# Optimization experiments

Hardware: AMD Instinct MI355X
Metric: run time of the kernel (lower is better)

The kernel has to match this reference:

```python
import jax, jax.numpy as jnp
import numpy as np

N, K, H, T = 65536, 8, 128, 4  # nodes, max children, h_size, n_types


def setup_inputs() -> dict:
    key = jax.random.key(0)
    ks = jax.random.split(key, 8)
    h = jax.random.normal(ks[0], (N, K, H), jnp.float32)          # mailbox child hidden states
    c = jax.random.normal(ks[1], (N, K, H), jnp.float32)          # mailbox child cell states
    f_input = jax.random.normal(ks[2], (N, H), jnp.float32)       # precomputed x @ W_f per node
    type_id = jax.random.randint(ks[3], (N,), 0, T, jnp.int32)    # node type for dispatch
    scale = 0.05
    U_iou = jax.random.normal(ks[4], (T, H, 3 * H), jnp.float32) * scale  # per-type i,o,u recurrent mats
    b_iou = jax.random.normal(ks[5], (T, 3 * H), jnp.float32) * scale
    U_f = jax.random.normal(ks[6], (T, H, H), jnp.float32) * scale        # per-type forget-gate mat
    b_f = jax.random.normal(ks[7], (T, H), jnp.float32) * scale
    return dict(h=h, c=c, f_input=f_input, type_id=type_id,
                U_iou=U_iou, b_iou=b_iou, U_f=U_f, b_f=b_f)


def reference(h, c, f_input, type_id, U_iou, b_iou, U_f, b_f):
    """TypedTreeCell.reduce_func: per-type TreeLSTM child aggregation.

    Returns concat([iou_aggr, c_aggr], -1) of shape [N, 4*H].
    """
    n_types = U_iou.shape[0]
    n_nodes = h.shape[0]
    h_size = h.shape[2]
    h_sum = h.sum(axis=1)  # [N, H] child-sum for i,o,u gates
    iou_aggr = jnp.zeros((n_nodes, 3 * h_size), h.dtype)
    c_aggr = jnp.zeros((n_nodes, h_size), h.dtype)
    for t in range(n_types):  # fixed small type loop mirrors the module's dispatch
        m = (type_id == t)[:, None]
        iou_t = h_sum @ U_iou[t] + b_iou[t]                                  # [N, 3H]
        f_t = jax.nn.sigmoid(f_input[:, None, :] + h @ U_f[t] + b_f[t])     # [N, K, H]
        c_t = (f_t * c).sum(axis=1)                                          # [N, H]
        iou_aggr = jnp.where(m, iou_t, iou_aggr)
        c_aggr = jnp.where(m, c_t, c_aggr)
    return jnp.concatenate([iou_aggr, c_aggr], axis=-1)
```

## Files before the change

kernel.cpp:

```cpp
#include <hip/hip_runtime.h>
#include <cstdint>


typedef __bf16 bf16;
typedef bf16 bf16x8 __attribute__((ext_vector_type(8)));
typedef bf16 bf16x4 __attribute__((ext_vector_type(4)));
typedef float f32x4 __attribute__((ext_vector_type(4)));

#define N_NODES 65536
#define KCH 8
#define HSZ 128
#define T_TYPES 4
#define TM 16
#define LDS_STRIDE 136

#define WS_PERM_OFF   256
#define WS_PREUF_OFF  (WS_PERM_OFF + 4*N_NODES)
#define WS_PREUIOU_OFF (WS_PREUF_OFF + 131072)

__global__ void k_count(const int* __restrict__ ta, int* __restrict__ ws_i) {
    int i = blockIdx.x * blockDim.x + threadIdx.x;
    int t = ta[i];
    int lane = threadIdx.x & 63;
    #pragma unroll
    for (int tt = 0; tt < T_TYPES; ++tt) {
        unsigned long long m = __ballot(t == tt);
        int leader = __ffsll((unsigned long long)m) - 1;
        if (t == tt && lane == leader)
            atomicAdd(&ws_i[tt], (int)__popcll(m));
    }
}

__global__ void k_offsets(int* ws_i) {
    if (threadIdx.x == 0 && blockIdx.x == 0) {
        int acc = 0, tacc = 0;
        for (int t = 0; t < T_TYPES; ++t) {
            int cnt = ws_i[t];
            ws_i[8 + t] = acc;
            ws_i[4 + t] = acc;
            ws_i[12 + t] = tacc;
            acc += cnt;
            tacc += (cnt + TM - 1) / TM;
        }
        ws_i[16] = tacc;
    }
}

__global__ void k_scatter(const int* __restrict__ ta, int* __restrict__ ws_i,
                          int* __restrict__ perm) {
    int i = blockIdx.x * blockDim.x + threadIdx.x;
    int t = ta[i];
    int lane = threadIdx.x & 63;
    #pragma unroll
    for (int tt = 0; tt < T_TYPES; ++tt) {
        unsigned long long m = __ballot(t == tt);
        if (t == tt) {
            int leader = __ffsll((unsigned long long)m) - 1;
            int base = 0;
            if (lane == leader) base = atomicAdd(&ws_i[4 + tt], (int)__popcll(m));
            base = __shfl(base, leader, 64);
            int rank = (int)__popcll(m & ((1ull << lane) - 1ull));
            perm[base + rank] = i;
        }
    }
}

__global__ void k_swz(const float* __restrict__ Uf, const float* __restrict__ Uiou,
                      bf16* __restrict__ dstf, bf16* __restrict__ dstiou) {
    int idx = blockIdx.x * blockDim.x + threadIdx.x;
    if (idx < T_TYPES * HSZ * HSZ) {
        int t = idx >> 14;
        int r = (idx >> 7) & 127;
        int j = idx & 127;
        float v = Uf[idx];
        int kblk = r >> 5, kin = r & 31;
        int lane = ((kin >> 3) << 4) | (j & 15);
        int e = kin & 7;
        int cb = j >> 4;
        dstf[((((t * 4 + kblk) * 8 + cb) * 64 + lane) << 3) + e] = (bf16)v;
    } else {
        int i2 = idx - T_TYPES * HSZ * HSZ;
        int t = i2 / 49152;
        int rm = i2 - t * 49152;
        int r = rm / 384;
        int j = rm - r * 384;
        float v = Uiou[i2];
        int kblk = r >> 5, kin = r & 31;
        int lane = ((kin >> 3) << 4) | (j & 15);
        int e = kin & 7;
        int cb = j >> 4;
        dstiou[((((t * 4 + kblk) * 24 + cb) * 64 + lane) << 3) + e] = (bf16)v;
    }
}

__global__ __launch_bounds__(512, 6) void k_main(
    const float* __restrict__ h, const float* __restrict__ c,
    const float* __restrict__ f_input,
    const float* __restrict__ b_iou, const float* __restrict__ b_f,
    const int* __restrict__ perm, const int* __restrict__ ws_i,
    const bf16* __restrict__ preUf, const bf16* __restrict__ preUiou,
    float* __restrict__ out)
{
    const int b = blockIdx.x;
    if (b >= ws_i[16]) return;
    int t;
    if (b < ws_i[13]) t = 0;
    else if (b < ws_i[14]) t = 1;
    else if (b < ws_i[15]) t = 2;
    else t = 3;
    const int tile = b - ws_i[12 + t];
    const int cnt = ws_i[t];
    const int base = ws_i[8 + t] + tile * TM;
    const int rem = min(TM, cnt - tile * TM);

    __shared__ __align__(16) bf16 hs[(128 + 16) * LDS_STRIDE];
    __shared__ int gn_lds[TM];
    bf16* hsum = hs + 128 * LDS_STRIDE;

    const int tid = threadIdx.x;
    const int w2 = tid >> 6;
    const int l = tid & 63;
    const int lu = l & 15;
    const int g = l >> 4;

    {
        int node = w2 * 2 + (g >> 1);
        int khalf = (g & 1) * 4;
        int mc = node < rem ? node : 0;
        int gn = perm[base + mc];
        if (lu == 0 && (g & 1) == 0) gn_lds[node] = gn;
        const float* hp = h + (long)gn * (KCH * HSZ) + lu * 8;
        float sarr[8];
        #pragma unroll
        for (int i = 0; i < 8; ++i) sarr[i] = 0.f;
        #pragma unroll
        for (int k0 = 0; k0 < 4; ++k0) {
            int k = khalf + k0;
            const float4* p = (const float4*)(hp + k * HSZ);
            float4 a = p[0], bb = p[1];
            sarr[0] += a.x; sarr[1] += a.y; sarr[2] += a.z; sarr[3] += a.w;
            sarr[4] += bb.x; sarr[5] += bb.y; sarr[6] += bb.z; sarr[7] += bb.w;
            bf16x8 v;
            v[0] = (bf16)a.x; v[1] = (bf16)a.y; v[2] = (bf16)a.z; v[3] = (bf16)a.w;
            v[4] = (bf16)bb.x; v[5] = (bf16)bb.y; v[6] = (bf16)bb.z; v[7] = (bf16)bb.w;
            *((bf16x8*)&hs[(node * KCH + k) * LDS_STRIDE + lu * 8]) = v;
        }
        #pragma unroll
        for (int i = 0; i < 8; ++i) sarr[i] += __shfl_xor(sarr[i], 16, 64);
        if ((g & 1) == 0) {
            bf16x8 sv;
            #pragma unroll
            for (int i = 0; i < 8; ++i) sv[i] = (bf16)sarr[i];
            *((bf16x8*)&hsum[node * LDS_STRIDE + lu * 8]) = sv;
        }
    }
    __syncthreads();

    f32x4 acc[4][2];
    #pragma unroll
    for (int rt = 0; rt < 4; ++rt)
        #pragma unroll
        for (int cb = 0; cb < 2; ++cb)
            acc[rt][cb] = (f32x4){0.f, 0.f, 0.f, 0.f};

    const int rbase = (w2 >> 2) * 4;
    const int cpair = (w2 & 3);
    const bf16x8* Bf = (const bf16x8*)preUf;
    #pragma unroll
    for (int kb = 0; kb < 4; ++kb) {
        bf16x8 b0 = Bf[((t * 4 + kb) * 8 + cpair * 2 + 0) * 64 + l];
        bf16x8 b1 = Bf[((t * 4 + kb) * 8 + cpair * 2 + 1) * 64 + l];
        #pragma unroll
        for (int rt = 0; rt < 4; ++rt) {
            bf16x8 a = *((const bf16x8*)&hs[((rbase + rt) * 16 + lu) * LDS_STRIDE + kb * 32 + g * 8]);
            acc[rt][0] = __builtin_amdgcn_mfma_f32_16x16x32_bf16(a, b0, acc[rt][0], 0, 0, 0);
            acc[rt][1] = __builtin_amdgcn_mfma_f32_16x16x32_bf16(a, b1, acc[rt][1], 0, 0, 0);
        }
    }

    f32x4 acc2[3];
    #pragma unroll
    for (int cf = 0; cf < 3; ++cf) acc2[cf] = (f32x4){0.f, 0.f, 0.f, 0.f};
    const bf16x8* Bi = (const bf16x8*)preUiou;
    #pragma unroll
    for (int kb = 0; kb < 4; ++kb) {
        bf16x8 a = *((const bf16x8*)&hsum[lu * LDS_STRIDE + kb * 32 + g * 8]);
        #pragma unroll
        for (int cf = 0; cf < 3; ++cf) {
            bf16x8 bfr = Bi[((t * 4 + kb) * 24 + w2 * 3 + cf) * 64 + l];
            acc2[cf] = __builtin_amdgcn_mfma_f32_16x16x32_bf16(a, bfr, acc2[cf], 0, 0, 0);
        }
    }

    {
        #pragma unroll
        for (int cf = 0; cf < 3; ++cf) {
            int col = (w2 * 3 + cf) * 16 + lu;
            float bi = b_iou[t * 384 + col];
            #pragma unroll
            for (int r = 0; r < 4; ++r) {
                int m = g * 4 + r;
                if (m < rem)
                    out[(long)gn_lds[m] * (4 * HSZ) + col] = acc2[cf][r] + bi;
            }
        }
    }

    {
        const int col0 = cpair * 32 + lu;
        const float bfv0 = b_f[t * HSZ + col0];
        const float bfv1 = b_f[t * HSZ + col0 + 16];
        const int ghalf = g >> 1;
        const int kbase = (g & 1) * 4;

        int nd[4]; bool ok2[4]; long gns2[4];
        #pragma unroll
        for (int rt = 0; rt < 4; ++rt) {
            nd[rt] = (rbase + rt) * 2 + ghalf;
            ok2[rt] = nd[rt] < rem;
            gns2[rt] = gn_lds[nd[rt]];
        }

        #pragma unroll
        for (int rt = 0; rt < 4; ++rt) {
            const float* fr = f_input + gns2[rt] * HSZ + col0;
            float fi0 = fr[0];
            float fi1 = fr[16];
            const float* crow = c + gns2[rt] * (long)(KCH * HSZ) + kbase * HSZ + col0;
            float cv0[4], cv1[4];
            #pragma unroll
            for (int r = 0; r < 4; ++r) {
                cv0[r] = crow[r * HSZ];
                cv1[r] = crow[r * HSZ + 16];
            }
            float p0 = 0.f, p1 = 0.f;
            #pragma unroll
            for (int r = 0; r < 4; ++r) {
                float s0 = acc[rt][0][r] + fi0 + bfv0;
                float s1 = acc[rt][1][r] + fi1 + bfv1;
                p0 += cv0[r] * __builtin_amdgcn_rcpf(1.f + __expf(-s0));
                p1 += cv1[r] * __builtin_amdgcn_rcpf(1.f + __expf(-s1));
            }
            p0 += __shfl_xor(p0, 16, 64);
            p1 += __shfl_xor(p1, 16, 64);
            if ((g & 1) == 0 && ok2[rt]) {
                float* orow = out + gns2[rt] * (4 * HSZ) + 3 * HSZ + col0;
                orow[0] = p0;
                orow[16] = p1;
            }
        }
    }
}

extern "C" void kernel_launch(void* const* d_in, const int* in_sizes, int n_in,
                              void* d_out, int out_size, void* d_ws, size_t ws_size,
                              hipStream_t stream) {
    const float* h       = (const float*)d_in[0];
    const float* c       = (const float*)d_in[1];
    const float* f_input = (const float*)d_in[2];
    const int*   type_id = (const int*)d_in[3];
    const float* U_iou   = (const float*)d_in[4];
    const float* b_iou   = (const float*)d_in[5];
    const float* U_f     = (const float*)d_in[6];
    const float* b_f     = (const float*)d_in[7];
    float* out = (float*)d_out;

    char* ws = (char*)d_ws;
    int* ws_i = (int*)ws;
    int* perm = (int*)(ws + WS_PERM_OFF);
    bf16* preUf = (bf16*)(ws + WS_PREUF_OFF);
    bf16* preUiou = (bf16*)(ws + WS_PREUIOU_OFF);

    hipMemsetAsync(ws, 0, 128, stream);
    k_swz    <<<(T_TYPES * HSZ * HSZ + T_TYPES * HSZ * 3 * HSZ) / 256, 256, 0, stream>>>(U_f, U_iou, preUf, preUiou);
    k_count  <<<N_NODES / 256, 256, 0, stream>>>(type_id, ws_i);
    k_offsets<<<1, 64, 0, stream>>>(ws_i);
    k_scatter<<<N_NODES / 256, 256, 0, stream>>>(type_id, ws_i, perm);

    k_main<<<N_NODES / TM + T_TYPES, 512, 0, stream>>>(h, c, f_input, b_iou, b_f,
                                                       perm, ws_i, preUf, preUiou, out);
}
```

Baseline: 713.5 us.

## Prefetch c and f_input early with double buffering, coalesce h loads

Issues the first c/f_input loads before the barrier and the second during the MFMA phase, then double-buffers the remaining c loads inside the gate epilogue so memory latency overlaps compute. h is now loaded as two 64-float halves per lane, giving contiguous per-row accesses, and is written to LDS as bf16x4 pairs. The final store is split across lane halves so both halves of the wave write. Launch bounds now request 8 blocks per CU instead of 6, which limits registers and may cause spills given the extra prefetch registers.

```diff
diff --git a/kernel.cpp b/kernel.cpp
--- a/kernel.cpp
+++ b/kernel.cpp
@@ -93,7 +93,7 @@
     }
 }
 
-__global__ __launch_bounds__(512, 6) void k_main(
+__global__ __launch_bounds__(512, 8) void k_main(
     const float* __restrict__ h, const float* __restrict__ c,
     const float* __restrict__ f_input,
     const float* __restrict__ b_iou, const float* __restrict__ b_f,
@@ -123,36 +123,58 @@
     const int lu = l & 15;
     const int g = l >> 4;
 
+    const int rbase = (w2 >> 2) * 4;
+    const int cpair = (w2 & 3);
+
     {
         int node = w2 * 2 + (g >> 1);
         int khalf = (g & 1) * 4;
         int mc = node < rem ? node : 0;
         int gn = perm[base + mc];
         if (lu == 0 && (g & 1) == 0) gn_lds[node] = gn;
-        const float* hp = h + (long)gn * (KCH * HSZ) + lu * 8;
+        const float* hp = h + (long)gn * (KCH * HSZ) + lu * 4;
         float sarr[8];
         #pragma unroll
         for (int i = 0; i < 8; ++i) sarr[i] = 0.f;
         #pragma unroll
         for (int k0 = 0; k0 < 4; ++k0) {
             int k = khalf + k0;
-            const float4* p = (const float4*)(hp + k * HSZ);
-            float4 a = p[0], bb = p[1];
+            float4 a  = *(const float4*)(hp + k * HSZ);
+            float4 bb = *(const float4*)(hp + k * HSZ + 64);
             sarr[0] += a.x; sarr[1] += a.y; sarr[2] += a.z; sarr[3] += a.w;
             sarr[4] += bb.x; sarr[5] += bb.y; sarr[6] += bb.z; sarr[7] += bb.w;
-            bf16x8 v;
-            v[0] = (bf16)a.x; v[1] = (bf16)a.y; v[2] = (bf16)a.z; v[3] = (bf16)a.w;
-            v[4] = (bf16)bb.x; v[5] = (bf16)bb.y; v[6] = (bf16)bb.z; v[7] = (bf16)bb.w;
-            *((bf16x8*)&hs[(node * KCH + k) * LDS_STRIDE + lu * 8]) = v;
+            bf16x4 v0, v1;
+            v0[0] = (bf16)a.x; v0[1] = (bf16)a.y; v0[2] = (bf16)a.z; v0[3] = (bf16)a.w;
+            v1[0] = (bf16)bb.x; v1[1] = (bf16)bb.y; v1[2] = (bf16)bb.z; v1[3] = (bf16)bb.w;
+            *((bf16x4*)&hs[(node * KCH + k) * LDS_STRIDE + lu * 4]) = v0;
+            *((bf16x4*)&hs[(node * KCH + k) * LDS_STRIDE + 64 + lu * 4]) = v1;
         }
         #pragma unroll
         for (int i = 0; i < 8; ++i) sarr[i] += __shfl_xor(sarr[i], 16, 64);
         if ((g & 1) == 0) {
-            bf16x8 sv;
-            #pragma unroll
-            for (int i = 0; i < 8; ++i) sv[i] = (bf16)sarr[i];
-            *((bf16x8*)&hsum[node * LDS_STRIDE + lu * 8]) = sv;
-        }
+            bf16x4 s0, s1;
+            s0[0] = (bf16)sarr[0]; s0[1] = (bf16)sarr[1]; s0[2] = (bf16)sarr[2]; s0[3] = (bf16)sarr[3];
+            s1[0] = (bf16)sarr[4]; s1[1] = (bf16)sarr[5]; s1[2] = (bf16)sarr[6]; s1[3] = (bf16)sarr[7];
+            *((bf16x4*)&hsum[node * LDS_STRIDE + lu * 4]) = s0;
+            *((bf16x4*)&hsum[node * LDS_STRIDE + 64 + lu * 4]) = s1;
+        }
+    }
+
+    const int col0 = cpair * 32 + lu;
+    const int kbase = (g & 1) * 4;
+    const int ghalf = g >> 1;
+    int gnE[4]; bool ok2[4];
+    #pragma unroll
+    for (int rt = 0; rt < 4; ++rt) {
+        int nd = (rbase + rt) * 2 + ghalf;
+        ok2[rt] = nd < rem;
+        gnE[rt] = perm[base + (ok2[rt] ? nd : 0)];
+    }
+    float cvv[2][4]; float fiv[2];
+    {
+        const float* cr = c + (long)gnE[0] * (KCH * HSZ) + kbase * HSZ + col0;
+        cvv[0][0] = cr[0]; cvv[0][1] = cr[HSZ]; cvv[0][2] = cr[2 * HSZ]; cvv[0][3] = cr[3 * HSZ];
+        fiv[0] = f_input[(long)gnE[0] * HSZ + col0];
     }
     __syncthreads();
 
@@ -163,8 +185,6 @@
         for (int cb = 0; cb < 2; ++cb)
             acc[rt][cb] = (f32x4){0.f, 0.f, 0.f, 0.f};
 
-    const int rbase = (w2 >> 2) * 4;
-    const int cpair = (w2 & 3);
     const bf16x8* Bf = (const bf16x8*)preUf;
     #pragma unroll
     for (int kb = 0; kb < 4; ++kb) {
@@ -176,6 +196,12 @@
             acc[rt][0] = __builtin_amdgcn_mfma_f32_16x16x32_bf16(a, b0, acc[rt][0], 0, 0, 0);
             acc[rt][1] = __builtin_amdgcn_mfma_f32_16x16x32_bf16(a, b1, acc[rt][1], 0, 0, 0);
         }
+    }
+
+    {
+        const float* cr = c + (long)gnE[0] * (KCH * HSZ) + kbase * HSZ + col0 + 16;
+        cvv[1][0] = cr[0]; cvv[1][1] = cr[HSZ]; cvv[1][2] = cr[2 * HSZ]; cvv[1][3] = cr[3 * HSZ];
+        fiv[1] = f_input[(long)gnE[0] * HSZ + col0 + 16];
     }
 
     f32x4 acc2[3];
@@ -207,46 +233,37 @@
     }
 
     {
-        const int col0 = cpair * 32 + lu;
-        const float bfv0 = b_f[t * HSZ + col0];
-        const float bfv1 = b_f[t * HSZ + col0 + 16];
-        const int ghalf = g >> 1;
-        const int kbase = (g & 1) * 4;
-
-        int nd[4]; bool ok2[4]; long gns2[4];
-        #pragma unroll
-        for (int rt = 0; rt < 4; ++rt) {
-            nd[rt] = (rbase + rt) * 2 + ghalf;
-            ok2[rt] = nd[rt] < rem;
-            gns2[rt] = gn_lds[nd[rt]];
-        }
-
-        #pragma unroll
-        for (int rt = 0; rt < 4; ++rt) {
-            const float* fr = f_input + gns2[rt] * HSZ + col0;
-            float fi0 = fr[0];
-            float fi1 = fr[16];
-            const float* crow = c + gns2[rt] * (long)(KCH * HSZ) + kbase * HSZ + col0;
-            float cv0[4], cv1[4];
+        const float bfc0 = b_f[t * HSZ + col0];
+        const float bfc1 = b_f[t * HSZ + col0 + 16];
+        float p0sav = 0.f;
+        #pragma unroll
+        for (int bi = 0; bi < 8; ++bi) {
+            const int rt = bi >> 1;
+            const int cb = bi & 1;
+            const int buf = bi & 1;
+            float fi = fiv[buf];
+            float bfv = cb ? bfc1 : bfc0;
+            float p = 0.f;
             #pragma unroll
             for (int r = 0; r < 4; ++r) {
-                cv0[r] = crow[r * HSZ];
-                cv1[r] = crow[r * HSZ + 16];
-            }
-            float p0 = 0.f, p1 = 0.f;
-            #pragma unroll
-            for (int r = 0; r < 4; ++r) {
-                float s0 = acc[rt][0][r] + fi0 + bfv0;
-                float s1 = acc[rt][1][r] + fi1 + bfv1;
-                p0 += cv0[r] * __builtin_amdgcn_rcpf(1.f + __expf(-s0));
-                p1 += cv1[r] * __builtin_amdgcn_rcpf(1.f + __expf(-s1));
-            }
-            p0 += __shfl_xor(p0, 16, 64);
-            p1 += __shfl_xor(p1, 16, 64);
-            if ((g & 1) == 0 && ok2[rt]) {
-                float* orow = out + gns2[rt] * (4 * HSZ) + 3 * HSZ + col0;
-                orow[0] = p0;
-                orow[16] = p1;
+                float s = acc[rt][cb][r] + fi + bfv;
+                p += cvv[buf][r] * __builtin_amdgcn_rcpf(1.f + __expf(-s));
+            }
+            if (bi < 6) {
+                const int nrt = (bi + 2) >> 1;
+                const int ncb = (bi + 2) & 1;
+                const float* cr = c + (long)gnE[nrt] * (KCH * HSZ) + kbase * HSZ + col0 + ncb * 16;
+                cvv[buf][0] = cr[0]; cvv[buf][1] = cr[HSZ];
+                cvv[buf][2] = cr[2 * HSZ]; cvv[buf][3] = cr[3 * HSZ];
+                fiv[buf] = f_input[(long)gnE[nrt] * HSZ + col0 + ncb * 16];
+            }
+            p += __shfl_xor(p, 16, 64);
+            if (cb == 0) {
+                p0sav = p;
+            } else {
+                float val = (g & 1) ? p : p0sav;
+                if (ok2[rt])
+                    out[(long)gnE[rt] * (4 * HSZ) + 3 * HSZ + cpair * 32 + (g & 1) * 16 + lu] = val;
             }
         }
     }
```

New measurement: 816.7 us. 1.14x slower.
